# Optimization experiments

Hardware: AMD Instinct MI355X
Metric: run time of the kernel (lower is better)

The kernel has to match this reference:

```python
import jax, jax.numpy as jnp
import numpy as np

# SLAYER neuron / simulation params (network.yaml defaults)
THETA = 10.0      # spike threshold
TAU_SR = 10.0     # PSP (SRM) kernel time constant
TAU_REF = 1.0     # refractory kernel time constant
SCALE_REF = 2.0   # refractory scale (x theta)
T_SAMPLE = 100    # simulation timesteps (tSample)
K_SRM = 100       # truncation length of SRM kernel
K_REF = 32        # truncation length of refractory kernel (tauRef=1 -> decays fast)


def srm_kernel():
    # eps(t) = (t/tau) * exp(1 - t/tau), t = 0..K_SRM-1
    t = jnp.arange(K_SRM, dtype=jnp.float32)
    return (t / TAU_SR) * jnp.exp(1.0 - t / TAU_SR)


def ref_kernel():
    # nu(t) = -scaleRef * theta * (t/tauRef) * exp(1 - t/tauRef), applied at t+1..t+K_REF
    t = jnp.arange(1, K_REF + 1, dtype=jnp.float32)
    return -SCALE_REF * THETA * (t / TAU_REF) * jnp.exp(1.0 - t / TAU_REF)


def psp(x):
    # causal temporal filter: y[t] = sum_k srm[k] * x[t-k]; x: (N, F, T)
    F = x.shape[1]
    k = srm_kernel()[::-1]                           # flip -> correlation == convolution
    w = jnp.broadcast_to(k, (F, 1, K_SRM))           # depthwise, same kernel each channel
    return jax.lax.conv_general_dilated(
        x, w, window_strides=(1,), padding=[(K_SRM - 1, 0)],
        dimension_numbers=('NCT', 'OIT', 'NCT'), feature_group_count=F)


def spike_fn(u):
    # hard threshold (forward math); amplitude 1/Ts = 1
    return (u >= THETA).astype(u.dtype)


def spike_layer(u):
    # u: (N, F, T) membrane potential. Sequential refractory feedback over time:
    # each spike injects the refractory kernel into the next K_REF timesteps.
    rk = ref_kernel()                                 # (K_REF,)
    u_t = jnp.moveaxis(u, -1, 0)                      # (T, N, F)
    buf0 = jnp.zeros(u.shape[:-1] + (K_REF,), u.dtype)

    def step(buf, ut):
        m = ut + buf[..., 0]                          # membrane incl. refractory
        s = spike_fn(m)
        buf = jnp.concatenate([buf[..., 1:], jnp.zeros_like(buf[..., :1])], axis=-1)
        buf = buf + s[..., None] * rk
        return buf, s

    _, sp = jax.lax.scan(step, buf0, u_t)             # sp: (T, N, F)
    return jnp.moveaxis(sp, 0, -1)                    # (N, F, T)


def setup_inputs() -> dict:
    key = jax.random.key(0)
    k1, k2, k3 = jax.random.split(key, 3)
    inp = jax.random.uniform(k1, (64, 3, 32, 32), dtype=jnp.float32)   # image-like input
    w1 = jax.random.normal(k2, (410, 3072), dtype=jnp.float32) * 0.5   # dense (32,32,3)->410
    w2 = jax.random.normal(k3, (10, 410), dtype=jnp.float32) * 0.5     # dense 410->10
    return {"input": inp, "w1": w1, "w2": w2}


def reference(input, w1, w2):
    N = input.shape[0]
    flat = input.reshape(N, -1)                               # (N, 3072)
    # replicate(): nearest-interp to T steps == broadcast over time
    x = jnp.broadcast_to(flat[..., None], flat.shape + (T_SAMPLE,))  # (N, 3072, T)
    a1 = jnp.einsum('nft,of->not', x, w1)                     # fc1 per timestep
    s1 = spike_layer(psp(a1))                                 # (N, 410, T)
    a2 = jnp.einsum('nft,of->not', s1, w2)                    # fc2 per timestep
    return spike_layer(psp(a2))                               # (N, 10, T)
```

## Files before the change

kernel.cpp:

```cpp
#include <hip/hip_runtime.h>

#define WS_PART   0
#define WS_SMASK  3407872
#define WS_A2     (WS_SMASK + 332800)

#define D_E1   2.71828182845904523536
#define D_EINV 0.36787944117144232160
#define D_G10  0.90483741803595957316
#define D_E10  0.27182818284590452354

__global__ __launch_bounds__(256) void k_gemm(const float* __restrict__ flat,
                                              const float* __restrict__ w1,
                                              float* __restrict__ partf) {
    __shared__ float tile[64 * 98];
    const int b   = blockIdx.x;
    const int s   = b & 31;
    const int og  = b >> 5;
    const int k0  = s * 96;
    const int tid = threadIdx.x;

    {
        const int row = tid >> 2, q = tid & 3;
        const float4* A4 = (const float4*)flat;
        const int gbase = row * 768 + s * 24 + q * 6;
        float* dst = &tile[row * 98 + q * 24];
#pragma unroll
        for (int i = 0; i < 6; ++i) {
            float4 v = A4[gbase + i];
            dst[i * 4 + 0] = v.x; dst[i * 4 + 1] = v.y;
            dst[i * 4 + 2] = v.z; dst[i * 4 + 3] = v.w;
        }
    }
    __syncthreads();

    const int w  = __builtin_amdgcn_readfirstlane(tid >> 6);
    const int o0 = og * 16 + w * 4;
    const int n  = tid & 63;

    double acc[4];
#pragma unroll
    for (int o = 0; o < 4; ++o) acc[o] = 0.0;

    const float* bp[4];
    bool valid[4];
#pragma unroll
    for (int o = 0; o < 4; ++o) {
        const int row = o0 + o;
        valid[o] = (row < 410);
        bp[o] = w1 + (size_t)(valid[o] ? row : 409) * 3072 + k0;
    }

#pragma unroll 4
    for (int kk = 0; kk < 96; kk += 8) {
        double ad[8];
        {
            float2 f0 = *(const float2*)&tile[n * 98 + kk + 0];
            float2 f1 = *(const float2*)&tile[n * 98 + kk + 2];
            float2 f2 = *(const float2*)&tile[n * 98 + kk + 4];
            float2 f3 = *(const float2*)&tile[n * 98 + kk + 6];
            ad[0] = (double)f0.x; ad[1] = (double)f0.y;
            ad[2] = (double)f1.x; ad[3] = (double)f1.y;
            ad[4] = (double)f2.x; ad[5] = (double)f2.y;
            ad[6] = (double)f3.x; ad[7] = (double)f3.y;
        }
#pragma unroll
        for (int o = 0; o < 4; ++o) {
            float4 ba = *(const float4*)(bp[o] + kk);
            float4 bb = *(const float4*)(bp[o] + kk + 4);
            acc[o] = fma(ad[0], (double)ba.x, acc[o]);
            acc[o] = fma(ad[1], (double)ba.y, acc[o]);
            acc[o] = fma(ad[2], (double)ba.z, acc[o]);
            acc[o] = fma(ad[3], (double)ba.w, acc[o]);
            acc[o] = fma(ad[4], (double)bb.x, acc[o]);
            acc[o] = fma(ad[5], (double)bb.y, acc[o]);
            acc[o] = fma(ad[6], (double)bb.z, acc[o]);
            acc[o] = fma(ad[7], (double)bb.w, acc[o]);
        }
    }

    float* prow = partf + (size_t)s * (416 * 64);
#pragma unroll
    for (int o = 0; o < 4; ++o)
        prow[(size_t)(o0 + o) * 64 + n] = valid[o] ? (float)acc[o] : 0.0f;
}

__global__ __launch_bounds__(256) void k_sim1(const float* __restrict__ partf,
                                              unsigned long long* __restrict__ smaskT2) {
    const int gid = blockIdx.x * 256 + threadIdx.x;
    const int f = gid >> 6, n = gid & 63;

    double a1 = 0.0;
#pragma unroll
    for (int s = 0; s < 32; ++s)
        a1 += (double)partf[((size_t)s * 416 + f) * 64 + n];

    double Et = D_E1, cs = 0.0, RA = 0.0, RB = 0.0;
    const bool l0 = (threadIdx.x & 63) == 0;

#pragma unroll 4
    for (int t = 0; t < 100; ++t) {
        cs = fma(0.1 * (double)t, Et, cs);
        double m = fma(a1, cs, RA);
        bool sp = (m >= 10.0);
        unsigned long long bl = __ballot(sp);
        if (l0) smaskT2[(size_t)t * 416 + f] = bl;
        double t1 = (RA + RB) * D_EINV;
        double t2 = RB * D_EINV;
        RA = sp ? t1 - 20.0 : t1;
        RB = sp ? t2 - 20.0 : t2;
        Et *= D_G10;
    }
}

__global__ __launch_bounds__(256) void k_fc2(const unsigned long long* __restrict__ smaskT2,
                                             const float* __restrict__ w2,
                                             double* __restrict__ a2s) {
    const int blk = blockIdx.x;
    const int o   = blk / 25;
    const int tq  = blk - o * 25;
    const int wi  = threadIdx.x >> 6;
    const int t   = __builtin_amdgcn_readfirstlane(tq * 4 + wi);
    const int n   = threadIdx.x & 63;

    const unsigned long long* mrow = smaskT2 + (size_t)t * 416;
    const float* wrow = w2 + o * 410;

    double c0 = 0.0, c1 = 0.0;
#pragma unroll 2
    for (int f0 = 0; f0 < 400; f0 += 20) {
        unsigned long long m[20];
        float wv[20];
#pragma unroll
        for (int i = 0; i < 20; ++i) { m[i] = mrow[f0 + i]; wv[i] = wrow[f0 + i]; }
#pragma unroll
        for (int i = 0; i < 20; ++i) {
            double bit = (double)((unsigned)((m[i] >> n) & 1ull));
            double wd  = (double)wv[i];
            if (i & 1) c1 = fma(bit, wd, c1);
            else       c0 = fma(bit, wd, c0);
        }
    }
    {
        unsigned long long m[10];
        float wv[10];
#pragma unroll
        for (int i = 0; i < 10; ++i) { m[i] = mrow[400 + i]; wv[i] = wrow[400 + i]; }
#pragma unroll
        for (int i = 0; i < 10; ++i) {
            double bit = (double)((unsigned)((m[i] >> n) & 1ull));
            double wd  = (double)wv[i];
            if (i & 1) c1 = fma(bit, wd, c1);
            else       c0 = fma(bit, wd, c0);
        }
    }
    a2s[((size_t)o * 100 + t) * 64 + n] = c0 + c1;
}

__global__ __launch_bounds__(64) void k_tail(const double* __restrict__ a2s,
                                             float* __restrict__ out) {
    const int o = blockIdx.x;
    const int n = threadIdx.x;
    const double* ap = a2s + (size_t)o * 6400 + n;
    float* orow = out + (size_t)n * 1000 + o * 100;

    double PA = 0.0, PB = 0.0, RA = 0.0, RB = 0.0;
#pragma unroll 1
    for (int tb = 0; tb < 4; ++tb) {
        double a[25];
#pragma unroll
        for (int i = 0; i < 25; ++i) a[i] = ap[(size_t)(tb * 25 + i) * 64];
#pragma unroll
        for (int i = 0; i < 25; ++i) {
            PB = fma(D_E10, a[i], PB);
            double m = PA + RA;
            bool sp = (m >= 10.0);
            orow[tb * 25 + i] = sp ? 1.0f : 0.0f;
            double p1 = (PA + PB) * D_G10;
            PB *= D_G10;
            PA = p1;
            double r1 = (RA + RB) * D_EINV;
            double r2 = RB * D_EINV;
            RA = sp ? r1 - 20.0 : r1;
            RB = sp ? r2 - 20.0 : r2;
        }
    }
}

extern "C" void kernel_launch(void* const* d_in, const int* in_sizes, int n_in,
                              void* d_out, int out_size, void* d_ws, size_t ws_size,
                              hipStream_t stream) {
    const float* input = (const float*)d_in[0];
    const float* w1    = (const float*)d_in[1];
    const float* w2    = (const float*)d_in[2];
    float* out = (float*)d_out;

    char* ws = (char*)d_ws;
    float* partf = (float*)(ws + WS_PART);
    unsigned long long* smaskT2 = (unsigned long long*)(ws + WS_SMASK);
    double* a2s  = (double*)(ws + WS_A2);

    k_gemm<<<832, 256, 0, stream>>>(input, w1, partf);
    k_sim1<<<104, 256, 0, stream>>>(partf, smaskT2);
    k_fc2 <<<250, 256, 0, stream>>>(smaskT2, w2, a2s);
    k_tail<<<10, 64, 0, stream>>>(a2s, out);
}
```

Baseline: 96.39 us.

## Fuse gemm with sim1 and fc2 with tail via last-block atomic counters

Merges the four kernel launches into two. Each pair uses a per-group atomic counter so that the last block to finish a group runs the dependent stage: the spike simulation for its 16 features, or the layer-2 tail for its output neuron. This is meant to remove launch gaps and the inter-kernel drain. The cost is a memset launch, fence and atomic overhead, and a serialized tail in which one block runs 4 features sequentially instead of spreading them across 104 blocks.

```diff
diff --git a/kernel.cpp b/kernel.cpp
--- a/kernel.cpp
+++ b/kernel.cpp
@@ -3,16 +3,20 @@
 #define WS_PART   0
 #define WS_SMASK  3407872
 #define WS_A2     (WS_SMASK + 332800)
+#define WS_CTR    (WS_A2 + 512000)
 
 #define D_E1   2.71828182845904523536
 #define D_EINV 0.36787944117144232160
 #define D_G10  0.90483741803595957316
 #define D_E10  0.27182818284590452354
 
-__global__ __launch_bounds__(256) void k_gemm(const float* __restrict__ flat,
-                                              const float* __restrict__ w1,
-                                              float* __restrict__ partf) {
+__global__ __launch_bounds__(256) void k_gemm_sim1(
+    const float* __restrict__ flat, const float* __restrict__ w1,
+    float* __restrict__ partf, unsigned* __restrict__ ctr,
+    unsigned long long* __restrict__ smaskT2)
+{
     __shared__ float tile[64 * 98];
+    __shared__ int lastFlag;
     const int b   = blockIdx.x;
     const int s   = b & 31;
     const int og  = b >> 5;
@@ -37,84 +41,96 @@
     const int o0 = og * 16 + w * 4;
     const int n  = tid & 63;
 
-    double acc[4];
-#pragma unroll
-    for (int o = 0; o < 4; ++o) acc[o] = 0.0;
-
-    const float* bp[4];
-    bool valid[4];
-#pragma unroll
-    for (int o = 0; o < 4; ++o) {
-        const int row = o0 + o;
-        valid[o] = (row < 410);
-        bp[o] = w1 + (size_t)(valid[o] ? row : 409) * 3072 + k0;
-    }
+    {
+        double acc[4];
+#pragma unroll
+        for (int o = 0; o < 4; ++o) acc[o] = 0.0;
+
+        const float* bp[4];
+        bool valid[4];
+#pragma unroll
+        for (int o = 0; o < 4; ++o) {
+            const int row = o0 + o;
+            valid[o] = (row < 410);
+            bp[o] = w1 + (size_t)(valid[o] ? row : 409) * 3072 + k0;
+        }
 
 #pragma unroll 4
-    for (int kk = 0; kk < 96; kk += 8) {
-        double ad[8];
-        {
-            float2 f0 = *(const float2*)&tile[n * 98 + kk + 0];
-            float2 f1 = *(const float2*)&tile[n * 98 + kk + 2];
-            float2 f2 = *(const float2*)&tile[n * 98 + kk + 4];
-            float2 f3 = *(const float2*)&tile[n * 98 + kk + 6];
-            ad[0] = (double)f0.x; ad[1] = (double)f0.y;
-            ad[2] = (double)f1.x; ad[3] = (double)f1.y;
-            ad[4] = (double)f2.x; ad[5] = (double)f2.y;
-            ad[6] = (double)f3.x; ad[7] = (double)f3.y;
-        }
-#pragma unroll
-        for (int o = 0; o < 4; ++o) {
-            float4 ba = *(const float4*)(bp[o] + kk);
-            float4 bb = *(const float4*)(bp[o] + kk + 4);
-            acc[o] = fma(ad[0], (double)ba.x, acc[o]);
-            acc[o] = fma(ad[1], (double)ba.y, acc[o]);
-            acc[o] = fma(ad[2], (double)ba.z, acc[o]);
-            acc[o] = fma(ad[3], (double)ba.w, acc[o]);
-            acc[o] = fma(ad[4], (double)bb.x, acc[o]);
-            acc[o] = fma(ad[5], (double)bb.y, acc[o]);
-            acc[o] = fma(ad[6], (double)bb.z, acc[o]);
-            acc[o] = fma(ad[7], (double)bb.w, acc[o]);
-        }
-    }
-
-    float* prow = partf + (size_t)s * (416 * 64);
-#pragma unroll
-    for (int o = 0; o < 4; ++o)
-        prow[(size_t)(o0 + o) * 64 + n] = valid[o] ? (float)acc[o] : 0.0f;
+        for (int kk = 0; kk < 96; kk += 8) {
+            double ad[8];
+            {
+                float2 f0 = *(const float2*)&tile[n * 98 + kk + 0];
+                float2 f1 = *(const float2*)&tile[n * 98 + kk + 2];
+                float2 f2 = *(const float2*)&tile[n * 98 + kk + 4];
+                float2 f3 = *(const float2*)&tile[n * 98 + kk + 6];
+                ad[0] = (double)f0.x; ad[1] = (double)f0.y;
+                ad[2] = (double)f1.x; ad[3] = (double)f1.y;
+                ad[4] = (double)f2.x; ad[5] = (double)f2.y;
+                ad[6] = (double)f3.x; ad[7] = (double)f3.y;
+            }
+#pragma unroll
+            for (int o = 0; o < 4; ++o) {
+                float4 ba = *(const float4*)(bp[o] + kk);
+                float4 bb = *(const float4*)(bp[o] + kk + 4);
+                acc[o] = fma(ad[0], (double)ba.x, acc[o]);
+                acc[o] = fma(ad[1], (double)ba.y, acc[o]);
+                acc[o] = fma(ad[2], (double)ba.z, acc[o]);
+                acc[o] = fma(ad[3], (double)ba.w, acc[o]);
+                acc[o] = fma(ad[4], (double)bb.x, acc[o]);
+                acc[o] = fma(ad[5], (double)bb.y, acc[o]);
+                acc[o] = fma(ad[6], (double)bb.z, acc[o]);
+                acc[o] = fma(ad[7], (double)bb.w, acc[o]);
+            }
+        }
+
+        float* prow = partf + (size_t)s * (416 * 64);
+#pragma unroll
+        for (int o = 0; o < 4; ++o)
+            prow[(size_t)(o0 + o) * 64 + n] = valid[o] ? (float)acc[o] : 0.0f;
+    }
+
+    __syncthreads();
+    if (tid == 0) {
+        __threadfence();
+        unsigned old = atomicAdd(&ctr[og], 1u);
+        lastFlag = (old == 31u);
+    }
+    __syncthreads();
+    if (!lastFlag) return;
+    __threadfence();
+
+    const bool l0 = (n == 0);
+#pragma unroll 1
+    for (int ff = 0; ff < 4; ++ff) {
+        const int f = og * 16 + w * 4 + ff;
+        double a1 = 0.0;
+#pragma unroll
+        for (int s2 = 0; s2 < 32; ++s2)
+            a1 += (double)partf[((size_t)s2 * 416 + f) * 64 + n];
+
+        double Et = D_E1, cs = 0.0, RA = 0.0, RB = 0.0;
+#pragma unroll 4
+        for (int t = 0; t < 100; ++t) {
+            cs = fma(0.1 * (double)t, Et, cs);
+            double m = fma(a1, cs, RA);
+            bool sp = (m >= 10.0);
+            unsigned long long bl = __ballot(sp);
+            if (l0) smaskT2[(size_t)t * 416 + f] = bl;
+            double t1 = (RA + RB) * D_EINV;
+            double t2 = RB * D_EINV;
+            RA = sp ? t1 - 20.0 : t1;
+            RB = sp ? t2 - 20.0 : t2;
+            Et *= D_G10;
+        }
+    }
 }
 
-__global__ __launch_bounds__(256) void k_sim1(const float* __restrict__ partf,
-                                              unsigned long long* __restrict__ smaskT2) {
-    const int gid = blockIdx.x * 256 + threadIdx.x;
-    const int f = gid >> 6, n = gid & 63;
-
-    double a1 = 0.0;
-#pragma unroll
-    for (int s = 0; s < 32; ++s)
-        a1 += (double)partf[((size_t)s * 416 + f) * 64 + n];
-
-    double Et = D_E1, cs = 0.0, RA = 0.0, RB = 0.0;
-    const bool l0 = (threadIdx.x & 63) == 0;
-
-#pragma unroll 4
-    for (int t = 0; t < 100; ++t) {
-        cs = fma(0.1 * (double)t, Et, cs);
-        double m = fma(a1, cs, RA);
-        bool sp = (m >= 10.0);
-        unsigned long long bl = __ballot(sp);
-        if (l0) smaskT2[(size_t)t * 416 + f] = bl;
-        double t1 = (RA + RB) * D_EINV;
-        double t2 = RB * D_EINV;
-        RA = sp ? t1 - 20.0 : t1;
-        RB = sp ? t2 - 20.0 : t2;
-        Et *= D_G10;
-    }
-}
-
-__global__ __launch_bounds__(256) void k_fc2(const unsigned long long* __restrict__ smaskT2,
-                                             const float* __restrict__ w2,
-                                             double* __restrict__ a2s) {
+__global__ __launch_bounds__(256) void k_fc2_tail(
+    const unsigned long long* __restrict__ smaskT2, const float* __restrict__ w2,
+    double* __restrict__ a2s, unsigned* __restrict__ ctr,
+    float* __restrict__ out)
+{
+    __shared__ int lastFlag;
     const int blk = blockIdx.x;
     const int o   = blk / 25;
     const int tq  = blk - o * 25;
@@ -122,44 +138,52 @@
     const int t   = __builtin_amdgcn_readfirstlane(tq * 4 + wi);
     const int n   = threadIdx.x & 63;
 
-    const unsigned long long* mrow = smaskT2 + (size_t)t * 416;
-    const float* wrow = w2 + o * 410;
-
-    double c0 = 0.0, c1 = 0.0;
+    {
+        const unsigned long long* mrow = smaskT2 + (size_t)t * 416;
+        const float* wrow = w2 + o * 410;
+
+        double c0 = 0.0, c1 = 0.0;
 #pragma unroll 2
-    for (int f0 = 0; f0 < 400; f0 += 20) {
-        unsigned long long m[20];
-        float wv[20];
-#pragma unroll
-        for (int i = 0; i < 20; ++i) { m[i] = mrow[f0 + i]; wv[i] = wrow[f0 + i]; }
-#pragma unroll
-        for (int i = 0; i < 20; ++i) {
-            double bit = (double)((unsigned)((m[i] >> n) & 1ull));
-            double wd  = (double)wv[i];
-            if (i & 1) c1 = fma(bit, wd, c1);
-            else       c0 = fma(bit, wd, c0);
-        }
-    }
-    {
-        unsigned long long m[10];
-        float wv[10];
-#pragma unroll
-        for (int i = 0; i < 10; ++i) { m[i] = mrow[400 + i]; wv[i] = wrow[400 + i]; }
-#pragma unroll
-        for (int i = 0; i < 10; ++i) {
-            double bit = (double)((unsigned)((m[i] >> n) & 1ull));
-            double wd  = (double)wv[i];
-            if (i & 1) c1 = fma(bit, wd, c1);
-            else       c0 = fma(bit, wd, c0);
-        }
-    }
-    a2s[((size_t)o * 100 + t) * 64 + n] = c0 + c1;
-}
-
-__global__ __launch_bounds__(64) void k_tail(const double* __restrict__ a2s,
-                                             float* __restrict__ out) {
-    const int o = blockIdx.x;
-    const int n = threadIdx.x;
+        for (int f0 = 0; f0 < 400; f0 += 20) {
+            unsigned long long m[20];
+            float wv[20];
+#pragma unroll
+            for (int i = 0; i < 20; ++i) { m[i] = mrow[f0 + i]; wv[i] = wrow[f0 + i]; }
+#pragma unroll
+            for (int i = 0; i < 20; ++i) {
+                double bit = (double)((unsigned)((m[i] >> n) & 1ull));
+                double wd  = (double)wv[i];
+                if (i & 1) c1 = fma(bit, wd, c1);
+                else       c0 = fma(bit, wd, c0);
+            }
+        }
+        {
+            unsigned long long m[10];
+            float wv[10];
+#pragma unroll
+            for (int i = 0; i < 10; ++i) { m[i] = mrow[400 + i]; wv[i] = wrow[400 + i]; }
+#pragma unroll
+            for (int i = 0; i < 10; ++i) {
+                double bit = (double)((unsigned)((m[i] >> n) & 1ull));
+                double wd  = (double)wv[i];
+                if (i & 1) c1 = fma(bit, wd, c1);
+                else       c0 = fma(bit, wd, c0);
+            }
+        }
+        a2s[((size_t)o * 100 + t) * 64 + n] = c0 + c1;
+    }
+
+    __syncthreads();
+    if (threadIdx.x == 0) {
+        __threadfence();
+        unsigned old = atomicAdd(&ctr[32 + o], 1u);
+        lastFlag = (old == 24u);
+    }
+    __syncthreads();
+    if (!lastFlag) return;
+    __threadfence();
+    if (threadIdx.x >= 64) return;
+
     const double* ap = a2s + (size_t)o * 6400 + n;
     float* orow = out + (size_t)n * 1000 + o * 100;
 
@@ -198,9 +222,9 @@
     float* partf = (float*)(ws + WS_PART);
     unsigned long long* smaskT2 = (unsigned long long*)(ws + WS_SMASK);
     double* a2s  = (double*)(ws + WS_A2);
-
-    k_gemm<<<832, 256, 0, stream>>>(input, w1, partf);
-    k_sim1<<<104, 256, 0, stream>>>(partf, smaskT2);
-    k_fc2 <<<250, 256, 0, stream>>>(smaskT2, w2, a2s);
-    k_tail<<<10, 64, 0, stream>>>(a2s, out);
+    unsigned* ctr = (unsigned*)(ws + WS_CTR);
+
+    hipMemsetAsync(ctr, 0, 256, stream);
+    k_gemm_sim1<<<832, 256, 0, stream>>>(input, w1, partf, ctr, smaskT2);
+    k_fc2_tail <<<250, 256, 0, stream>>>(smaskT2, w2, a2s, ctr, out);
 }
```

New measurement: 180.8 us. 87.6% more time.
